# Performance work log

Hardware: AMD Instinct MI355X
Metric: run time of the kernel (lower is better)

Reference implementation:

```python
import jax, jax.numpy as jnp
import numpy as np
from jax import lax

B, V, M, C, CM, D = 48, 16, 32, 48, 8, 128
VOCAB_V, VOCAB_M, OUT = 2000, 1000, 256


def setup_inputs() -> dict:
    key = jax.random.key(0)
    ks = jax.random.split(key, 22)
    s = 0.1  # keep GRU gates out of saturation
    return {
        "visit_ids": jax.random.randint(ks[0], (3, B, V, C), 0, VOCAB_V),
        "mon_ids": jax.random.randint(ks[1], (4, B, V, M, CM), 0, VOCAB_M),
        "weight_vals": jax.random.uniform(ks[2], (B, V)),
        "age_vals": jax.random.uniform(ks[3], (B, V)),
        "emb_visit": jax.random.normal(ks[4], (3, VOCAB_V, D)) * s,
        "emb_mon": jax.random.normal(ks[5], (4, VOCAB_M, D)) * s,
        "mgru_Wih": jax.random.normal(ks[6], (5, 3 * D, D)) * s,
        "mgru_Whh": jax.random.normal(ks[7], (5, 3 * D, D)) * s,
        "mgru_bih": jax.random.normal(ks[8], (5, 3 * D)) * s,
        "mgru_bhh": jax.random.normal(ks[9], (5, 3 * D)) * s,
        "vgru_Wih": jax.random.normal(ks[10], (7, 3 * D, D)) * s,
        "vgru_Whh": jax.random.normal(ks[11], (7, 3 * D, D)) * s,
        "vgru_bih": jax.random.normal(ks[12], (7, 3 * D)) * s,
        "vgru_bhh": jax.random.normal(ks[13], (7, 3 * D)) * s,
        "fc_weight_w": jax.random.normal(ks[14], (D, 1)) * s,
        "fc_weight_b": jax.random.normal(ks[15], (D,)) * s,
        "fc_age_w": jax.random.normal(ks[16], (D, 1)) * s,
        "fc_age_b": jax.random.normal(ks[17], (D,)) * s,
        "fc_out_w": jax.random.normal(ks[18], (OUT, 7 * D)) * s,
        "fc_out_b": jax.random.normal(ks[19], (OUT,)) * s,
    }


def gru_last(x, Wih, Whh, bih, bhh):
    """torch.nn.GRU(batch_first=True), return final hidden [N, D]."""
    xi = jnp.einsum('ntd,ed->nte', x, Wih) + bih  # [N, T, 3D] input projections
    h0 = jnp.zeros((x.shape[0], Whh.shape[1]), x.dtype)

    def step(h, gi):
        gh = h @ Whh.T + bhh
        ir, iz, inn = jnp.split(gi, 3, axis=-1)
        hr, hz, hn = jnp.split(gh, 3, axis=-1)
        r = jax.nn.sigmoid(ir + hr)
        z = jax.nn.sigmoid(iz + hz)
        n = jnp.tanh(inn + r * hn)
        return (1.0 - z) * n + z * h, None

    hT, _ = lax.scan(step, h0, jnp.swapaxes(xi, 0, 1))
    return hT


def reference(visit_ids, mon_ids, weight_vals, age_vals, emb_visit, emb_mon,
              mgru_Wih, mgru_Whh, mgru_bih, mgru_bhh,
              vgru_Wih, vgru_Whh, vgru_bih, vgru_bhh,
              fc_weight_w, fc_weight_b, fc_age_w, fc_age_b,
              fc_out_w, fc_out_b):
    # padding_idx=0 -> zero embedding row (dropout in eval mode = identity)
    ev = emb_visit.at[:, 0].set(0.0)
    em = emb_mon.at[:, 0].set(0.0)

    # visit-event embedding-bag: sum over code dim -> [B, V, D] per feature
    visit_origin = [jnp.sum(ev[k][visit_ids[k]], axis=2) for k in range(3)]

    def run_stream(t, mi, vi):
        # monitor-level GRU over M, then visit-level GRU over V
        h1 = gru_last(t, mgru_Wih[mi], mgru_Whh[mi], mgru_bih[mi], mgru_bhh[mi])
        h2 = gru_last(h1.reshape(B, V, D),
                      vgru_Wih[vi], vgru_Whh[vi], vgru_bih[vi], vgru_bhh[vi])
        return h2  # [B, D]

    # output slots in dict-insertion order: lab_item, cond, proc, drug, inj_item, weight, age
    slots = [None] * 7
    for p in range(2):  # (lab_item, lab_value), (inj_item, inj_value)
        # elementwise item*value embedding, summed over codes -> [B*V, M, D]
        mon = jnp.sum(em[2 * p][mon_ids[2 * p]] * em[2 * p + 1][mon_ids[2 * p + 1]],
                      axis=3).reshape(B * V, M, D)
        slots[0 if p == 0 else 4] = run_stream(mon, p, p)
        for k in range(3):  # visit features repeated along monitor dim
            t = jnp.broadcast_to(visit_origin[k][:, :, None, :],
                                 (B, V, M, D)).reshape(B * V, M, D)
            h = run_stream(t, 2 + k, 2 + k)
            slots[1 + k] = h if slots[1 + k] is None else slots[1 + k] + h

    # weight / age: Linear(1->D), zero-mask, visit-level GRU
    for vals, w, b, vi, slot in ((weight_vals, fc_weight_w, fc_weight_b, 5, 5),
                                 (age_vals, fc_age_w, fc_age_b, 6, 6)):
        xf = vals.reshape(-1, 1)
        h = (xf @ w.T + b) * (xf != 0)
        slots[slot] = gru_last(h.reshape(B, V, D),
                               vgru_Wih[vi], vgru_Whh[vi], vgru_bih[vi], vgru_bhh[vi])

    patient_emb = jnp.concatenate(slots, axis=-1)  # [B, 7D]
    return jax.nn.relu(patient_emb) @ fc_out_w.T + fc_out_b
```

## Files before the change

### kernel.cpp

```cpp
#include <hip/hip_runtime.h>
#include <stdint.h>


typedef unsigned short u16;
typedef uint32_t u32;
typedef short bf8 __attribute__((ext_vector_type(8)));
typedef float f4 __attribute__((ext_vector_type(4)));

static __device__ __forceinline__ float bf2f(u16 b){ u32 u=((u32)b)<<16; float f; __builtin_memcpy(&f,&u,4); return f; }
static __device__ __forceinline__ u16 f2bf(float f){ u32 u; __builtin_memcpy(&u,&f,4); u32 r=(u+0x7fffu+((u>>16)&1u))>>16; return (u16)r; }
static __device__ __forceinline__ float bflo(u32 u){ u32 x=u<<16; float f; __builtin_memcpy(&f,&x,4); return f; }
static __device__ __forceinline__ float bfhi(u32 u){ u32 x=u&0xffff0000u; float f; __builtin_memcpy(&f,&x,4); return f; }
static __device__ __forceinline__ f4 mfma16(bf8 a, bf8 b, f4 c){ return __builtin_amdgcn_mfma_f32_16x16x32_bf16(a,b,c,0,0,0); }

#if __has_builtin(__builtin_amdgcn_exp2f)
static __device__ __forceinline__ float fexp2(float x){ return __builtin_amdgcn_exp2f(x); }
#else
static __device__ __forceinline__ float fexp2(float x){ float r; asm volatile("v_exp_f32 %0, %1" : "=v"(r) : "v"(x)); return r; }
#endif
#if __has_builtin(__builtin_amdgcn_rcpf)
static __device__ __forceinline__ float frcp(float x){ return __builtin_amdgcn_rcpf(x); }
#else
static __device__ __forceinline__ float frcp(float x){ float r; asm volatile("v_rcp_f32 %0, %1" : "=v"(r) : "v"(x)); return r; }
#endif

#define LOG2E 1.44269504089f
static __device__ __forceinline__ float sigm(float x){ return frcp(1.0f + fexp2(-LOG2E*x)); }
static __device__ __forceinline__ float tanh_f(float x){ return 1.0f - 2.0f*frcp(1.0f + fexp2((2.0f*LOG2E)*x)); }

__global__ __launch_bounds__(256) void k_prep(const float* __restrict__ s0, const float* __restrict__ s1,
                                              const float* __restrict__ s2, const float* __restrict__ s3,
                                              const float* __restrict__ s4,
                                              u16* __restrict__ d0, u16* __restrict__ d1,
                                              u16* __restrict__ d2, u16* __restrict__ d3,
                                              u16* __restrict__ d4){
  int y = blockIdx.y;
  const float* src = y==0?s0 : y==1?s1 : y==2?s2 : y==3?s3 : s4;
  u16* dst         = y==0?d0 : y==1?d1 : y==2?d2 : y==3?d3 : d4;
  int n4 = (y<2 ? 245760 : y<4 ? 344064 : 512000) >> 2;
  int i = blockIdx.x*256 + threadIdx.x;
  if (i < n4){
    float4 v = *(const float4*)(src + (size_t)i*4);
    ushort4 o = { f2bf(v.x), f2bf(v.y), f2bf(v.z), f2bf(v.w) };
    *(ushort4*)(dst + (size_t)i*4) = o;
  }
}

__global__ __launch_bounds__(128) void k_front(const int* __restrict__ vids,
                                               const float* __restrict__ embv,
                                               const float* __restrict__ wv, const float* __restrict__ av,
                                               const float* __restrict__ ww, const float* __restrict__ wb,
                                               const float* __restrict__ aw, const float* __restrict__ ab,
                                               u16* __restrict__ vis_org, u16* __restrict__ hin2T){
  __shared__ int ids[48];
  int y = blockIdx.y, row = blockIdx.x, d = threadIdx.x;
  if (y < 3){
    if (d < 48) ids[d] = vids[((size_t)y*768 + row)*48 + d];
    __syncthreads();
    const float* eb = embv + (size_t)y*2000*128;
    float acc = 0.f;
    #pragma unroll 4
    for (int c = 0; c < 48; ++c){ int id = ids[c]; if (id) acc += eb[(size_t)id*128 + d]; }
    vis_org[((size_t)y*768 + row)*128 + d] = f2bf(acc);
  } else {
    int sidx = y - 3;
    const float* vals = sidx ? av : wv;
    const float* wgt  = sidx ? aw : ww;
    const float* bias = sidx ? ab : wb;
    float v = vals[row];
    float h = (v != 0.f) ? (v * wgt[d] + bias[d]) : 0.f;
    int b = row >> 4, vv = row & 15;
    hin2T[((size_t)(5+sidx)*768 + (size_t)vv*48 + b)*128 + d] = f2bf(h);
  }
}

__global__ __launch_bounds__(256) void k_embed_mon(const int* __restrict__ mids,
                                                   const u16* __restrict__ embm_b,
                                                   u16* __restrict__ mon_xT){
  int p = blockIdx.y;
  int rid = threadIdx.x >> 5, lane32 = threadIdx.x & 31, d0 = lane32*4;
  __shared__ int ids[8][16];
  if (threadIdx.x < 128){
    int rr = threadIdx.x >> 4, c = threadIdx.x & 15;
    int f = 2*p + (c>>3), cm = c & 7;
    ids[rr][c] = mids[((size_t)f*24576 + (size_t)blockIdx.x*8 + rr)*8 + cm];
  }
  __syncthreads();
  const u16* e1 = embm_b + (size_t)(2*p)*1000*128;
  const u16* e2 = embm_b + (size_t)(2*p+1)*1000*128;
  float a0=0.f,a1=0.f,a2=0.f,a3=0.f;
  #pragma unroll
  for (int c = 0; c < 8; ++c){
    int i1 = ids[rid][c], i2 = ids[rid][8+c];
    if (i1 && i2){
      uint2 a = *(const uint2*)(e1 + (size_t)i1*128 + d0);
      uint2 b = *(const uint2*)(e2 + (size_t)i2*128 + d0);
      a0 += bflo(a.x)*bflo(b.x); a1 += bfhi(a.x)*bfhi(b.x);
      a2 += bflo(a.y)*bflo(b.y); a3 += bfhi(a.y)*bfhi(b.y);
    }
  }
  size_t nm = (size_t)blockIdx.x*8 + rid;
  int bv = (int)(nm >> 5), m = (int)(nm & 31);
  ushort4 o = { f2bf(a0), f2bf(a1), f2bf(a2), f2bf(a3) };
  *(ushort4*)(mon_xT + (size_t)p*24576*128 + ((size_t)m*768 + bv)*128 + d0) = o;
}


#define BARRIER() asm volatile("s_waitcnt lgkmcnt(0)\n\ts_barrier" ::: "memory")

#define ALOAD(D, tt) { int t_=(tt); if (t_>=T) t_=0; \
  const u16* p_ = ap + (size_t)t_*rstride; \
  D[0]=*(const bf8*)(p_); D[1]=*(const bf8*)(p_+32); \
  D[2]=*(const bf8*)(p_+64); D[3]=*(const bf8*)(p_+96); }

#define GIMM(G0,G1,G2,D) { \
  f4 t0_={biv[0],biv[0],biv[0],biv[0]}; G0=t0_; \
  f4 t1_={biv[1],biv[1],biv[1],biv[1]}; G1=t1_; \
  f4 t2_={biv[2],biv[2],biv[2],biv[2]}; G2=t2_; \
  G0=mfma16(D[0],wfi[0][0],G0); G0=mfma16(D[1],wfi[0][1],G0); \
  G0=mfma16(D[2],wfi[0][2],G0); G0=mfma16(D[3],wfi[0][3],G0); \
  G1=mfma16(D[0],wfi[1][0],G1); G1=mfma16(D[1],wfi[1][1],G1); \
  G1=mfma16(D[2],wfi[1][2],G1); G1=mfma16(D[3],wfi[1][3],G1); \
  G2=mfma16(D[0],wfi[2][0],G2); G2=mfma16(D[1],wfi[2][1],G2); \
  G2=mfma16(D[2],wfi[2][2],G2); G2=mfma16(D[3],wfi[2][3],G2); }

#define GHRD() \
  bf8 hf0_=*(const bf8*)&hlds[cur][lr][lq*8]; \
  bf8 hf1_=*(const bf8*)&hlds[cur][lr][32+lq*8]; \
  bf8 hf2_=*(const bf8*)&hlds[cur][lr][64+lq*8]; \
  bf8 hf3_=*(const bf8*)&hlds[cur][lr][96+lq*8]; \
  f4 a0_={bhv[0],bhv[0],bhv[0],bhv[0]}; \
  f4 a1_={bhv[1],bhv[1],bhv[1],bhv[1]}; \
  f4 a2_={bhv[2],bhv[2],bhv[2],bhv[2]}; \
  a0_=mfma16(hf0_,wfh[0][0],a0_); a0_=mfma16(hf1_,wfh[0][1],a0_); \
  a0_=mfma16(hf2_,wfh[0][2],a0_); a0_=mfma16(hf3_,wfh[0][3],a0_); \
  a1_=mfma16(hf0_,wfh[1][0],a1_); a1_=mfma16(hf1_,wfh[1][1],a1_); \
  a1_=mfma16(hf2_,wfh[1][2],a1_); a1_=mfma16(hf3_,wfh[1][3],a1_); \
  a2_=mfma16(hf0_,wfh[2][0],a2_); a2_=mfma16(hf1_,wfh[2][1],a2_); \
  a2_=mfma16(hf2_,wfh[2][2],a2_); a2_=mfma16(hf3_,wfh[2][3],a2_);

#define GATES(G0,G1,G2) { int nxt_=cur^1; \
  _Pragma("unroll") \
  for (int r=0;r<4;++r){ \
    float rr_=sigm(G0[r]+a0_[r]); \
    float zz_=sigm(G1[r]+a1_[r]); \
    float nn_=tanh_f(G2[r]+rr_*a2_[r]); \
    float hv_=(1.0f-zz_)*nn_+zz_*hp[r]; hp[r]=hv_; \
    hlds[nxt_][lq*4+r][w*16+lr]=f2bf(hv_); } \
  BARRIER(); cur=nxt_; }

#define STEP0(G0,G1,G2) { \
  f4 a0_={bhv[0],bhv[0],bhv[0],bhv[0]}; \
  f4 a1_={bhv[1],bhv[1],bhv[1],bhv[1]}; \
  f4 a2_={bhv[2],bhv[2],bhv[2],bhv[2]}; \
  GATES(G0,G1,G2); }

#define STEPB(G0,G1,G2,SN,tt) { \
  GHRD(); \
  GATES(G0,G1,G2); \
  if ((tt)+2 < T){ GIMM(G0,G1,G2,SN); } \
  ALOAD(SN,(tt)+4); }

__global__ __launch_bounds__(512, 2) void k_gru(int mode,
    const u16* __restrict__ Asrc, const u16* __restrict__ Asrc2,
    const u16* __restrict__ Wih, const float* __restrict__ bih,
    const u16* __restrict__ Whh, const float* __restrict__ bhh,
    u16* __restrict__ hout, int T){
  int s = blockIdx.y, g = blockIdx.x;
  const u16* A; size_t rstride; u16* ho; int widx;
  if (mode == 0){
    if (s < 2){ A = Asrc + (size_t)s*24576*128; rstride = 768*128; }
    else      { A = Asrc2 + (size_t)(s-2)*768*128; rstride = 0; }
    widx = s;
    int slot = (0x32140u >> (4*s)) & 15;
    ho = hout + (size_t)slot*768*128;
  } else {
    A = Asrc + (size_t)s*768*128; rstride = 48*128;
    widx = (0x6514320u >> (4*s)) & 15;
    ho = hout + (size_t)s*48*128;
  }
  const u16* Wi = Wih + (size_t)widx*384*128;
  const u16* Wh = Whh + (size_t)widx*384*128;
  const float* bi = bih + (size_t)widx*384;
  const float* bh = bhh + (size_t)widx*384;

  int w = threadIdx.x >> 6, l = threadIdx.x & 63;
  int lr = l & 15, lq = l >> 4;

  bf8 wfi[3][4], wfh[3][4]; float biv[3], bhv[3];
  #pragma unroll
  for (int j = 0; j < 3; ++j){
    int colb = (w + 8*j)*16;
    const u16* wpi = Wi + (size_t)(colb + lr)*128 + lq*8;
    const u16* wph = Wh + (size_t)(colb + lr)*128 + lq*8;
    #pragma unroll
    for (int kt = 0; kt < 4; ++kt){
      wfi[j][kt] = *(const bf8*)(wpi + kt*32);
      wfh[j][kt] = *(const bf8*)(wph + kt*32);
    }
    biv[j] = bi[colb + lr];
    bhv[j] = bh[colb + lr];
  }

  const u16* ap = A + (size_t)(g*16 + lr)*128 + lq*8;
  __shared__ u16 hlds[2][16][132];
  float hp[4] = {0.f,0.f,0.f,0.f};
  int cur = 0;

  if (rstride){
    bf8 S0[4], S1[4];
    f4 gE0,gE1,gE2, gO0,gO1,gO2;
    ALOAD(S0,0); ALOAD(S1,1);
    GIMM(gE0,gE1,gE2,S0); ALOAD(S0,2);
    GIMM(gO0,gO1,gO2,S1); ALOAD(S1,3);
    STEP0(gE0,gE1,gE2);
    GIMM(gE0,gE1,gE2,S0); ALOAD(S0,4);
    STEPB(gO0,gO1,gO2,S1,1);
    for (int t = 2; t < T; t += 2){
      STEPB(gE0,gE1,gE2,S0,t);
      STEPB(gO0,gO1,gO2,S1,t+1);
    }
  } else {
    bf8 S0[4];
    f4 gE0,gE1,gE2;
    ALOAD(S0,0);
    GIMM(gE0,gE1,gE2,S0);
    STEP0(gE0,gE1,gE2);
    for (int t = 1; t < T; ++t){
      GHRD();
      GATES(gE0,gE1,gE2);
    }
  }

  if (mode == 0){
    #pragma unroll
    for (int r = 0; r < 4; ++r)
      ho[((size_t)(lq*4+r)*48 + g)*128 + w*16 + lr] = f2bf(hp[r]);
  } else {
    #pragma unroll
    for (int r = 0; r < 4; ++r)
      ho[((size_t)(g*16 + lq*4 + r))*128 + w*16 + lr] = f2bf(hp[r]);
  }
}

__global__ __launch_bounds__(256) void k_final(const u16* __restrict__ h2,
                                               const float* __restrict__ W,
                                               const float* __restrict__ Bias,
                                               float* __restrict__ out){
  int b = blockIdx.x, t = threadIdx.x;
  __shared__ float emb[896];
  for (int i = t; i < 896; i += 256){
    int j = i >> 7, d = i & 127;
    float v = bf2f(h2[((size_t)j*48 + b)*128 + d]);
    if (j >= 1 && j <= 3) v *= 2.0f;
    emb[i] = fmaxf(v, 0.f);
  }
  __syncthreads();
  float acc = Bias[t];
  const float* wp = W + (size_t)t*896;
  for (int i = 0; i < 896; i += 8){
    float4 w0 = *(const float4*)(wp + i);
    float4 w1 = *(const float4*)(wp + i + 4);
    acc += w0.x*emb[i]   + w0.y*emb[i+1] + w0.z*emb[i+2] + w0.w*emb[i+3];
    acc += w1.x*emb[i+4] + w1.y*emb[i+5] + w1.z*emb[i+6] + w1.w*emb[i+7];
  }
  out[(size_t)b*256 + t] = acc;
}

extern "C" void kernel_launch(void* const* d_in, const int* in_sizes, int n_in,
                              void* d_out, int out_size, void* d_ws, size_t ws_size,
                              hipStream_t stream){
  const int*   visit_ids   = (const int*)d_in[0];
  const int*   mon_ids     = (const int*)d_in[1];
  const float* weight_vals = (const float*)d_in[2];
  const float* age_vals    = (const float*)d_in[3];
  const float* emb_visit   = (const float*)d_in[4];
  const float* emb_mon     = (const float*)d_in[5];
  const float* mgru_Wih    = (const float*)d_in[6];
  const float* mgru_Whh    = (const float*)d_in[7];
  const float* mgru_bih    = (const float*)d_in[8];
  const float* mgru_bhh    = (const float*)d_in[9];
  const float* vgru_Wih    = (const float*)d_in[10];
  const float* vgru_Whh    = (const float*)d_in[11];
  const float* vgru_bih    = (const float*)d_in[12];
  const float* vgru_bhh    = (const float*)d_in[13];
  const float* fc_w_w      = (const float*)d_in[14];
  const float* fc_w_b      = (const float*)d_in[15];
  const float* fc_a_w      = (const float*)d_in[16];
  const float* fc_a_b      = (const float*)d_in[17];
  const float* fc_out_w    = (const float*)d_in[18];
  const float* fc_out_b    = (const float*)d_in[19];

  char* ws = (char*)d_ws;
  size_t o = 0;
  u16* mWih_b  = (u16*)(ws+o); o += 5ull*384*128*2;
  u16* mWhh_b  = (u16*)(ws+o); o += 5ull*384*128*2;
  u16* vWih_b  = (u16*)(ws+o); o += 7ull*384*128*2;
  u16* vWhh_b  = (u16*)(ws+o); o += 7ull*384*128*2;
  u16* embm_b  = (u16*)(ws+o); o += 4ull*1000*128*2;
  u16* mon_xT  = (u16*)(ws+o); o += 2ull*24576*128*2;
  u16* vis_org = (u16*)(ws+o); o += 3ull*768*128*2;
  u16* hin2T   = (u16*)(ws+o); o += 7ull*768*128*2;
  u16* h2      = (u16*)(ws+o); o += 7ull*48*128*2;

  k_prep<<<dim3(500,5), 256, 0, stream>>>(mgru_Wih, mgru_Whh, vgru_Wih, vgru_Whh, emb_mon,
                                          mWih_b, mWhh_b, vWih_b, vWhh_b, embm_b);
  k_front<<<dim3(768,5), 128, 0, stream>>>(visit_ids, emb_visit,
                                           weight_vals, age_vals, fc_w_w, fc_w_b, fc_a_w, fc_a_b,
                                           vis_org, hin2T);
  k_embed_mon<<<dim3(3072,2), 256, 0, stream>>>(mon_ids, embm_b, mon_xT);
  k_gru<<<dim3(48,5), 512, 0, stream>>>(0, mon_xT, vis_org,
                                        mWih_b, mgru_bih, mWhh_b, mgru_bhh, hin2T, 32);
  k_gru<<<dim3(3,7), 512, 0, stream>>>(1, hin2T, (const u16*)0,
                                       vWih_b, vgru_bih, vWhh_b, vgru_bhh, h2, 16);
  k_final<<<48, 256, 0, stream>>>(h2, fc_out_w, fc_out_b, (float*)d_out);
}
```

Before: 132.9 us.

## Fuse front-end kernels and interleave two GRU groups per block

Merges the weight-conversion, visit-embedding, scalar-feature and monitor-embedding kernels into one launch. The monitor embedding now reads fp32 tables directly instead of first writing a bf16 copy. Each GRU block now advances two independent 16-row recurrences in lockstep, so the MFMA and transcendental latency of one chain can hide behind the other. The weight and age visit-level GRUs also run inside the first GRU launch rather than waiting for the second. The cost is half as many GRU blocks, more registers per block, and duplicated work when the last group index is clamped.

```diff
diff --git a/kernel.cpp b/kernel.cpp
--- a/kernel.cpp
+++ b/kernel.cpp
@@ -9,8 +9,6 @@
 
 static __device__ __forceinline__ float bf2f(u16 b){ u32 u=((u32)b)<<16; float f; __builtin_memcpy(&f,&u,4); return f; }
 static __device__ __forceinline__ u16 f2bf(float f){ u32 u; __builtin_memcpy(&u,&f,4); u32 r=(u+0x7fffu+((u>>16)&1u))>>16; return (u16)r; }
-static __device__ __forceinline__ float bflo(u32 u){ u32 x=u<<16; float f; __builtin_memcpy(&f,&x,4); return f; }
-static __device__ __forceinline__ float bfhi(u32 u){ u32 x=u&0xffff0000u; float f; __builtin_memcpy(&f,&x,4); return f; }
 static __device__ __forceinline__ f4 mfma16(bf8 a, bf8 b, f4 c){ return __builtin_amdgcn_mfma_f32_16x16x32_bf16(a,b,c,0,0,0); }
 
 #if __has_builtin(__builtin_amdgcn_exp2f)
@@ -23,166 +21,183 @@
 #else
 static __device__ __forceinline__ float frcp(float x){ float r; asm volatile("v_rcp_f32 %0, %1" : "=v"(r) : "v"(x)); return r; }
 #endif
-
 #define LOG2E 1.44269504089f
 static __device__ __forceinline__ float sigm(float x){ return frcp(1.0f + fexp2(-LOG2E*x)); }
 static __device__ __forceinline__ float tanh_f(float x){ return 1.0f - 2.0f*frcp(1.0f + fexp2((2.0f*LOG2E)*x)); }
 
-__global__ __launch_bounds__(256) void k_prep(const float* __restrict__ s0, const float* __restrict__ s1,
-                                              const float* __restrict__ s2, const float* __restrict__ s3,
-                                              const float* __restrict__ s4,
-                                              u16* __restrict__ d0, u16* __restrict__ d1,
-                                              u16* __restrict__ d2, u16* __restrict__ d3,
-                                              u16* __restrict__ d4){
+__global__ __launch_bounds__(256) void k_pre(const int* __restrict__ vids, const int* __restrict__ mids,
+    const float* __restrict__ embv, const float* __restrict__ embm,
+    const float* __restrict__ wv, const float* __restrict__ av,
+    const float* __restrict__ ww, const float* __restrict__ wb,
+    const float* __restrict__ aw, const float* __restrict__ ab,
+    const float* __restrict__ mWih_f, const float* __restrict__ mWhh_f,
+    const float* __restrict__ vWih_f, const float* __restrict__ vWhh_f,
+    u16* __restrict__ mWih_b, u16* __restrict__ mWhh_b,
+    u16* __restrict__ vWih_b, u16* __restrict__ vWhh_b,
+    u16* __restrict__ mon_xT, u16* __restrict__ vis_org, u16* __restrict__ hin2T){
   int y = blockIdx.y;
-  const float* src = y==0?s0 : y==1?s1 : y==2?s2 : y==3?s3 : s4;
-  u16* dst         = y==0?d0 : y==1?d1 : y==2?d2 : y==3?d3 : d4;
-  int n4 = (y<2 ? 245760 : y<4 ? 344064 : 512000) >> 2;
-  int i = blockIdx.x*256 + threadIdx.x;
-  if (i < n4){
-    float4 v = *(const float4*)(src + (size_t)i*4);
+  if (y < 2){
+    int p = y;
+    int rid = threadIdx.x >> 5, lane32 = threadIdx.x & 31, d0 = lane32*4;
+    __shared__ int ids[8][16];
+    if (threadIdx.x < 128){
+      int rr = threadIdx.x >> 4, c = threadIdx.x & 15;
+      int f = 2*p + (c>>3), cm = c & 7;
+      ids[rr][c] = mids[((size_t)f*24576 + (size_t)blockIdx.x*8 + rr)*8 + cm];
+    }
+    __syncthreads();
+    const float* e1 = embm + (size_t)(2*p)*1000*128;
+    const float* e2 = embm + (size_t)(2*p+1)*1000*128;
+    float a0=0.f,a1=0.f,a2=0.f,a3=0.f;
+    #pragma unroll
+    for (int c = 0; c < 8; ++c){
+      int i1 = ids[rid][c], i2 = ids[rid][8+c];
+      if (i1 && i2){
+        float4 a = *(const float4*)(e1 + (size_t)i1*128 + d0);
+        float4 b = *(const float4*)(e2 + (size_t)i2*128 + d0);
+        a0 += a.x*b.x; a1 += a.y*b.y; a2 += a.z*b.z; a3 += a.w*b.w;
+      }
+    }
+    size_t nm = (size_t)blockIdx.x*8 + rid;
+    int bv = (int)(nm >> 5), m = (int)(nm & 31);
+    ushort4 o = { f2bf(a0), f2bf(a1), f2bf(a2), f2bf(a3) };
+    *(ushort4*)(mon_xT + (size_t)p*24576*128 + ((size_t)m*768 + bv)*128 + d0) = o;
+  } else if (y == 2){
+    int i = blockIdx.x*256 + threadIdx.x;
+    if (i >= 294912) return;
+    const float* s; u16* d; int off;
+    if (i < 61440)      { s = mWih_f; d = mWih_b; off = i; }
+    else if (i < 122880){ s = mWhh_f; d = mWhh_b; off = i - 61440; }
+    else if (i < 208896){ s = vWih_f; d = vWih_b; off = i - 122880; }
+    else                { s = vWhh_f; d = vWhh_b; off = i - 208896; }
+    float4 v = *(const float4*)(s + (size_t)off*4);
     ushort4 o = { f2bf(v.x), f2bf(v.y), f2bf(v.z), f2bf(v.w) };
-    *(ushort4*)(dst + (size_t)i*4) = o;
+    *(ushort4*)(d + (size_t)off*4) = o;
+  } else {
+    int x = blockIdx.x;
+    int sub = threadIdx.x >> 7, d = threadIdx.x & 127;
+    if (x < 1152){
+      __shared__ int ids[2][48];
+      int row = x*2 + sub;
+      int k = row / 768, bv = row - k*768;
+      if (d < 48) ids[sub][d] = vids[((size_t)k*768 + bv)*48 + d];
+      __syncthreads();
+      const float* eb = embv + (size_t)k*2000*128;
+      float acc = 0.f;
+      #pragma unroll 4
+      for (int c = 0; c < 48; ++c){ int id = ids[sub][c]; if (id) acc += eb[(size_t)id*128 + d]; }
+      vis_org[((size_t)k*768 + bv)*128 + d] = f2bf(acc);
+    } else if (x < 1920){
+      int grow = (x - 1152)*2 + sub;
+      int sidx = grow >= 768 ? 1 : 0;
+      int row = grow - sidx*768;
+      const float* vals = sidx ? av : wv;
+      const float* wgt  = sidx ? aw : ww;
+      const float* bias = sidx ? ab : wb;
+      float v = vals[row];
+      float h = (v != 0.f) ? (v * wgt[d] + bias[d]) : 0.f;
+      int b = row >> 4, vv = row & 15;
+      hin2T[((size_t)(5+sidx)*768 + (size_t)vv*48 + b)*128 + d] = f2bf(h);
+    }
   }
 }
 
-__global__ __launch_bounds__(128) void k_front(const int* __restrict__ vids,
-                                               const float* __restrict__ embv,
-                                               const float* __restrict__ wv, const float* __restrict__ av,
-                                               const float* __restrict__ ww, const float* __restrict__ wb,
-                                               const float* __restrict__ aw, const float* __restrict__ ab,
-                                               u16* __restrict__ vis_org, u16* __restrict__ hin2T){
-  __shared__ int ids[48];
-  int y = blockIdx.y, row = blockIdx.x, d = threadIdx.x;
-  if (y < 3){
-    if (d < 48) ids[d] = vids[((size_t)y*768 + row)*48 + d];
-    __syncthreads();
-    const float* eb = embv + (size_t)y*2000*128;
-    float acc = 0.f;
-    #pragma unroll 4
-    for (int c = 0; c < 48; ++c){ int id = ids[c]; if (id) acc += eb[(size_t)id*128 + d]; }
-    vis_org[((size_t)y*768 + row)*128 + d] = f2bf(acc);
-  } else {
-    int sidx = y - 3;
-    const float* vals = sidx ? av : wv;
-    const float* wgt  = sidx ? aw : ww;
-    const float* bias = sidx ? ab : wb;
-    float v = vals[row];
-    float h = (v != 0.f) ? (v * wgt[d] + bias[d]) : 0.f;
-    int b = row >> 4, vv = row & 15;
-    hin2T[((size_t)(5+sidx)*768 + (size_t)vv*48 + b)*128 + d] = f2bf(h);
-  }
-}
-
-__global__ __launch_bounds__(256) void k_embed_mon(const int* __restrict__ mids,
-                                                   const u16* __restrict__ embm_b,
-                                                   u16* __restrict__ mon_xT){
-  int p = blockIdx.y;
-  int rid = threadIdx.x >> 5, lane32 = threadIdx.x & 31, d0 = lane32*4;
-  __shared__ int ids[8][16];
-  if (threadIdx.x < 128){
-    int rr = threadIdx.x >> 4, c = threadIdx.x & 15;
-    int f = 2*p + (c>>3), cm = c & 7;
-    ids[rr][c] = mids[((size_t)f*24576 + (size_t)blockIdx.x*8 + rr)*8 + cm];
-  }
-  __syncthreads();
-  const u16* e1 = embm_b + (size_t)(2*p)*1000*128;
-  const u16* e2 = embm_b + (size_t)(2*p+1)*1000*128;
-  float a0=0.f,a1=0.f,a2=0.f,a3=0.f;
-  #pragma unroll
-  for (int c = 0; c < 8; ++c){
-    int i1 = ids[rid][c], i2 = ids[rid][8+c];
-    if (i1 && i2){
-      uint2 a = *(const uint2*)(e1 + (size_t)i1*128 + d0);
-      uint2 b = *(const uint2*)(e2 + (size_t)i2*128 + d0);
-      a0 += bflo(a.x)*bflo(b.x); a1 += bfhi(a.x)*bfhi(b.x);
-      a2 += bflo(a.y)*bflo(b.y); a3 += bfhi(a.y)*bfhi(b.y);
-    }
-  }
-  size_t nm = (size_t)blockIdx.x*8 + rid;
-  int bv = (int)(nm >> 5), m = (int)(nm & 31);
-  ushort4 o = { f2bf(a0), f2bf(a1), f2bf(a2), f2bf(a3) };
-  *(ushort4*)(mon_xT + (size_t)p*24576*128 + ((size_t)m*768 + bv)*128 + d0) = o;
-}
-
 
 #define BARRIER() asm volatile("s_waitcnt lgkmcnt(0)\n\ts_barrier" ::: "memory")
 
-#define ALOAD(D, tt) { int t_=(tt); if (t_>=T) t_=0; \
+#define ALOADg(S, ap, tt) { int t_=(tt); if (t_>=T) t_=0; \
   const u16* p_ = ap + (size_t)t_*rstride; \
-  D[0]=*(const bf8*)(p_); D[1]=*(const bf8*)(p_+32); \
-  D[2]=*(const bf8*)(p_+64); D[3]=*(const bf8*)(p_+96); }
-
-#define GIMM(G0,G1,G2,D) { \
+  S[0]=*(const bf8*)(p_); S[1]=*(const bf8*)(p_+32); \
+  S[2]=*(const bf8*)(p_+64); S[3]=*(const bf8*)(p_+96); }
+
+#define GIMMg(G0,G1,G2,S) { \
   f4 t0_={biv[0],biv[0],biv[0],biv[0]}; G0=t0_; \
   f4 t1_={biv[1],biv[1],biv[1],biv[1]}; G1=t1_; \
   f4 t2_={biv[2],biv[2],biv[2],biv[2]}; G2=t2_; \
-  G0=mfma16(D[0],wfi[0][0],G0); G0=mfma16(D[1],wfi[0][1],G0); \
-  G0=mfma16(D[2],wfi[0][2],G0); G0=mfma16(D[3],wfi[0][3],G0); \
-  G1=mfma16(D[0],wfi[1][0],G1); G1=mfma16(D[1],wfi[1][1],G1); \
-  G1=mfma16(D[2],wfi[1][2],G1); G1=mfma16(D[3],wfi[1][3],G1); \
-  G2=mfma16(D[0],wfi[2][0],G2); G2=mfma16(D[1],wfi[2][1],G2); \
-  G2=mfma16(D[2],wfi[2][2],G2); G2=mfma16(D[3],wfi[2][3],G2); }
-
-#define GHRD() \
-  bf8 hf0_=*(const bf8*)&hlds[cur][lr][lq*8]; \
-  bf8 hf1_=*(const bf8*)&hlds[cur][lr][32+lq*8]; \
-  bf8 hf2_=*(const bf8*)&hlds[cur][lr][64+lq*8]; \
-  bf8 hf3_=*(const bf8*)&hlds[cur][lr][96+lq*8]; \
-  f4 a0_={bhv[0],bhv[0],bhv[0],bhv[0]}; \
-  f4 a1_={bhv[1],bhv[1],bhv[1],bhv[1]}; \
-  f4 a2_={bhv[2],bhv[2],bhv[2],bhv[2]}; \
-  a0_=mfma16(hf0_,wfh[0][0],a0_); a0_=mfma16(hf1_,wfh[0][1],a0_); \
-  a0_=mfma16(hf2_,wfh[0][2],a0_); a0_=mfma16(hf3_,wfh[0][3],a0_); \
-  a1_=mfma16(hf0_,wfh[1][0],a1_); a1_=mfma16(hf1_,wfh[1][1],a1_); \
-  a1_=mfma16(hf2_,wfh[1][2],a1_); a1_=mfma16(hf3_,wfh[1][3],a1_); \
-  a2_=mfma16(hf0_,wfh[2][0],a2_); a2_=mfma16(hf1_,wfh[2][1],a2_); \
-  a2_=mfma16(hf2_,wfh[2][2],a2_); a2_=mfma16(hf3_,wfh[2][3],a2_);
-
-#define GATES(G0,G1,G2) { int nxt_=cur^1; \
+  G0=mfma16(S[0],wfi[0][0],G0); G0=mfma16(S[1],wfi[0][1],G0); \
+  G0=mfma16(S[2],wfi[0][2],G0); G0=mfma16(S[3],wfi[0][3],G0); \
+  G1=mfma16(S[0],wfi[1][0],G1); G1=mfma16(S[1],wfi[1][1],G1); \
+  G1=mfma16(S[2],wfi[1][2],G1); G1=mfma16(S[3],wfi[1][3],G1); \
+  G2=mfma16(S[0],wfi[2][0],G2); G2=mfma16(S[1],wfi[2][1],G2); \
+  G2=mfma16(S[2],wfi[2][2],G2); G2=mfma16(S[3],wfi[2][3],G2); }
+
+#define GHRDg(a0,a1,a2,grp) { \
+  bf8 hf0_=*(const bf8*)&hlds[cur][grp][lr][lq*8]; \
+  bf8 hf1_=*(const bf8*)&hlds[cur][grp][lr][32+lq*8]; \
+  bf8 hf2_=*(const bf8*)&hlds[cur][grp][lr][64+lq*8]; \
+  bf8 hf3_=*(const bf8*)&hlds[cur][grp][lr][96+lq*8]; \
+  f4 i0_={bhv[0],bhv[0],bhv[0],bhv[0]}; a0=i0_; \
+  f4 i1_={bhv[1],bhv[1],bhv[1],bhv[1]}; a1=i1_; \
+  f4 i2_={bhv[2],bhv[2],bhv[2],bhv[2]}; a2=i2_; \
+  a0=mfma16(hf0_,wfh[0][0],a0); a0=mfma16(hf1_,wfh[0][1],a0); \
+  a0=mfma16(hf2_,wfh[0][2],a0); a0=mfma16(hf3_,wfh[0][3],a0); \
+  a1=mfma16(hf0_,wfh[1][0],a1); a1=mfma16(hf1_,wfh[1][1],a1); \
+  a1=mfma16(hf2_,wfh[1][2],a1); a1=mfma16(hf3_,wfh[1][3],a1); \
+  a2=mfma16(hf0_,wfh[2][0],a2); a2=mfma16(hf1_,wfh[2][1],a2); \
+  a2=mfma16(hf2_,wfh[2][2],a2); a2=mfma16(hf3_,wfh[2][3],a2); }
+
+#define GATESg(G0,G1,G2,a0,a1,a2,hp,grp,nxt) { \
   _Pragma("unroll") \
   for (int r=0;r<4;++r){ \
-    float rr_=sigm(G0[r]+a0_[r]); \
-    float zz_=sigm(G1[r]+a1_[r]); \
-    float nn_=tanh_f(G2[r]+rr_*a2_[r]); \
+    float rr_=sigm(G0[r]+a0[r]); \
+    float zz_=sigm(G1[r]+a1[r]); \
+    float nn_=tanh_f(G2[r]+rr_*a2[r]); \
     float hv_=(1.0f-zz_)*nn_+zz_*hp[r]; hp[r]=hv_; \
-    hlds[nxt_][lq*4+r][w*16+lr]=f2bf(hv_); } \
+    hlds[nxt][grp][lq*4+r][w*16+lr]=f2bf(hv_); } }
+
+#define STEP0P() { int nxt_=cur^1; \
+  f4 aA0={bhv[0],bhv[0],bhv[0],bhv[0]}, aA1={bhv[1],bhv[1],bhv[1],bhv[1]}, aA2={bhv[2],bhv[2],bhv[2],bhv[2]}; \
+  f4 aB0=aA0, aB1=aA1, aB2=aA2; \
+  GATESg(eA0,eA1,eA2,aA0,aA1,aA2,hpA,0,nxt_); \
+  GATESg(eB0,eB1,eB2,aB0,aB1,aB2,hpB,1,nxt_); \
   BARRIER(); cur=nxt_; }
 
-#define STEP0(G0,G1,G2) { \
-  f4 a0_={bhv[0],bhv[0],bhv[0],bhv[0]}; \
-  f4 a1_={bhv[1],bhv[1],bhv[1],bhv[1]}; \
-  f4 a2_={bhv[2],bhv[2],bhv[2],bhv[2]}; \
-  GATES(G0,G1,G2); }
-
-#define STEPB(G0,G1,G2,SN,tt) { \
-  GHRD(); \
-  GATES(G0,G1,G2); \
-  if ((tt)+2 < T){ GIMM(G0,G1,G2,SN); } \
-  ALOAD(SN,(tt)+4); }
-
-__global__ __launch_bounds__(512, 2) void k_gru(int mode,
-    const u16* __restrict__ Asrc, const u16* __restrict__ Asrc2,
-    const u16* __restrict__ Wih, const float* __restrict__ bih,
-    const u16* __restrict__ Whh, const float* __restrict__ bhh,
-    u16* __restrict__ hout, int T){
-  int s = blockIdx.y, g = blockIdx.x;
-  const u16* A; size_t rstride; u16* ho; int widx;
-  if (mode == 0){
-    if (s < 2){ A = Asrc + (size_t)s*24576*128; rstride = 768*128; }
-    else      { A = Asrc2 + (size_t)(s-2)*768*128; rstride = 0; }
-    widx = s;
+#define STEPP(GA0,GA1,GA2,GB0,GB1,GB2,tt) { int nxt_=cur^1; \
+  f4 aA0,aA1,aA2,aB0,aB1,aB2; \
+  GHRDg(aA0,aA1,aA2,0); \
+  GHRDg(aB0,aB1,aB2,1); \
+  GATESg(GA0,GA1,GA2,aA0,aA1,aA2,hpA,0,nxt_); \
+  GATESg(GB0,GB1,GB2,aB0,aB1,aB2,hpB,1,nxt_); \
+  BARRIER(); cur=nxt_; \
+  if ((tt)+2 < T){ GIMMg(GA0,GA1,GA2,SA); GIMMg(GB0,GB1,GB2,SB); } \
+  ALOADg(SA,apA,(tt)+3); ALOADg(SB,apB,(tt)+3); }
+
+#define STEPC() { int nxt_=cur^1; \
+  f4 aA0,aA1,aA2,aB0,aB1,aB2; \
+  GHRDg(aA0,aA1,aA2,0); \
+  GHRDg(aB0,aB1,aB2,1); \
+  GATESg(eA0,eA1,eA2,aA0,aA1,aA2,hpA,0,nxt_); \
+  GATESg(eB0,eB1,eB2,aB0,aB1,aB2,hpB,1,nxt_); \
+  BARRIER(); cur=nxt_; }
+
+__global__ __launch_bounds__(512, 2) void k_gru(int phase,
+    const u16* __restrict__ mon_xT, const u16* __restrict__ vis_org,
+    u16* __restrict__ hin2T, u16* __restrict__ h2,
+    const u16* __restrict__ mWih, const float* __restrict__ mbih,
+    const u16* __restrict__ mWhh, const float* __restrict__ mbhh,
+    const u16* __restrict__ vWih, const float* __restrict__ vbih,
+    const u16* __restrict__ vWhh, const float* __restrict__ vbhh){
+  int s = blockIdx.y;
+  const u16* A; size_t rstride; int T, oMode, gA, gB;
+  const u16 *Wi, *Wh; const float *bi2, *bh2; u16* ho;
+  bool vjob = (phase == 1) || (s >= 5);
+  if (!vjob){
+    T = 32; oMode = 0; gA = 2*blockIdx.x; gB = gA + 1;
+    if (s < 2){ A = mon_xT + (size_t)s*24576*128; rstride = 768*128; }
+    else      { A = vis_org + (size_t)(s-2)*768*128; rstride = 0; }
+    Wi = mWih + (size_t)s*49152; Wh = mWhh + (size_t)s*49152;
+    bi2 = mbih + (size_t)s*384;  bh2 = mbhh + (size_t)s*384;
     int slot = (0x32140u >> (4*s)) & 15;
-    ho = hout + (size_t)slot*768*128;
+    ho = hin2T + (size_t)slot*768*128;
   } else {
-    A = Asrc + (size_t)s*768*128; rstride = 48*128;
-    widx = (0x6514320u >> (4*s)) & 15;
-    ho = hout + (size_t)s*48*128;
-  }
-  const u16* Wi = Wih + (size_t)widx*384*128;
-  const u16* Wh = Whh + (size_t)widx*384*128;
-  const float* bi = bih + (size_t)widx*384;
-  const float* bh = bhh + (size_t)widx*384;
+    if (blockIdx.x >= 2) return;
+    T = 16; oMode = 1; gA = 2*blockIdx.x; gB = gA + 1; if (gB > 2) gB = 2;
+    A = hin2T + (size_t)s*768*128; rstride = 48*128;
+    int vi = (0x6514320u >> (4*s)) & 15;
+    Wi = vWih + (size_t)vi*49152; Wh = vWhh + (size_t)vi*49152;
+    bi2 = vbih + (size_t)vi*384;  bh2 = vbhh + (size_t)vi*384;
+    ho = h2 + (size_t)s*48*128;
+  }
 
   int w = threadIdx.x >> 6, l = threadIdx.x & 63;
   int lr = l & 15, lq = l >> 4;
@@ -198,48 +213,53 @@
       wfi[j][kt] = *(const bf8*)(wpi + kt*32);
       wfh[j][kt] = *(const bf8*)(wph + kt*32);
     }
-    biv[j] = bi[colb + lr];
-    bhv[j] = bh[colb + lr];
-  }
-
-  const u16* ap = A + (size_t)(g*16 + lr)*128 + lq*8;
-  __shared__ u16 hlds[2][16][132];
-  float hp[4] = {0.f,0.f,0.f,0.f};
+    biv[j] = bi2[colb + lr];
+    bhv[j] = bh2[colb + lr];
+  }
+
+  const u16* apA = A + (size_t)(gA*16 + lr)*128 + lq*8;
+  const u16* apB = A + (size_t)(gB*16 + lr)*128 + lq*8;
+  __shared__ u16 hlds[2][2][16][132];
+  float hpA[4] = {0.f,0.f,0.f,0.f}, hpB[4] = {0.f,0.f,0.f,0.f};
   int cur = 0;
 
   if (rstride){
-    bf8 S0[4], S1[4];
-    f4 gE0,gE1,gE2, gO0,gO1,gO2;
-    ALOAD(S0,0); ALOAD(S1,1);
-    GIMM(gE0,gE1,gE2,S0); ALOAD(S0,2);
-    GIMM(gO0,gO1,gO2,S1); ALOAD(S1,3);
-    STEP0(gE0,gE1,gE2);
-    GIMM(gE0,gE1,gE2,S0); ALOAD(S0,4);
-    STEPB(gO0,gO1,gO2,S1,1);
+    bf8 SA[4], SB[4];
+    f4 eA0,eA1,eA2, oA0,oA1,oA2, eB0,eB1,eB2, oB0,oB1,oB2;
+    ALOADg(SA,apA,0); ALOADg(SB,apB,0);
+    GIMMg(eA0,eA1,eA2,SA); GIMMg(eB0,eB1,eB2,SB);
+    ALOADg(SA,apA,1); ALOADg(SB,apB,1);
+    GIMMg(oA0,oA1,oA2,SA); GIMMg(oB0,oB1,oB2,SB);
+    ALOADg(SA,apA,2); ALOADg(SB,apB,2);
+    STEP0P();
+    GIMMg(eA0,eA1,eA2,SA); GIMMg(eB0,eB1,eB2,SB);
+    ALOADg(SA,apA,3); ALOADg(SB,apB,3);
+    STEPP(oA0,oA1,oA2,oB0,oB1,oB2,1);
     for (int t = 2; t < T; t += 2){
-      STEPB(gE0,gE1,gE2,S0,t);
-      STEPB(gO0,gO1,gO2,S1,t+1);
+      STEPP(eA0,eA1,eA2,eB0,eB1,eB2,t);
+      STEPP(oA0,oA1,oA2,oB0,oB1,oB2,t+1);
     }
   } else {
-    bf8 S0[4];
-    f4 gE0,gE1,gE2;
-    ALOAD(S0,0);
-    GIMM(gE0,gE1,gE2,S0);
-    STEP0(gE0,gE1,gE2);
-    for (int t = 1; t < T; ++t){
-      GHRD();
-      GATES(gE0,gE1,gE2);
-    }
-  }
-
-  if (mode == 0){
+    bf8 SA[4], SB[4];
+    f4 eA0,eA1,eA2, eB0,eB1,eB2;
+    ALOADg(SA,apA,0); ALOADg(SB,apB,0);
+    GIMMg(eA0,eA1,eA2,SA); GIMMg(eB0,eB1,eB2,SB);
+    STEP0P();
+    for (int t = 1; t < T; ++t) STEPC();
+  }
+
+  if (oMode == 0){
     #pragma unroll
-    for (int r = 0; r < 4; ++r)
-      ho[((size_t)(lq*4+r)*48 + g)*128 + w*16 + lr] = f2bf(hp[r]);
+    for (int r = 0; r < 4; ++r){
+      ho[((size_t)(lq*4+r)*48 + gA)*128 + w*16 + lr] = f2bf(hpA[r]);
+      ho[((size_t)(lq*4+r)*48 + gB)*128 + w*16 + lr] = f2bf(hpB[r]);
+    }
   } else {
     #pragma unroll
-    for (int r = 0; r < 4; ++r)
-      ho[((size_t)(g*16 + lq*4 + r))*128 + w*16 + lr] = f2bf(hp[r]);
+    for (int r = 0; r < 4; ++r){
+      ho[((size_t)(gA*16 + lq*4 + r))*128 + w*16 + lr] = f2bf(hpA[r]);
+      ho[((size_t)(gB*16 + lq*4 + r))*128 + w*16 + lr] = f2bf(hpB[r]);
+    }
   }
 }
 
@@ -297,21 +317,19 @@
   u16* mWhh_b  = (u16*)(ws+o); o += 5ull*384*128*2;
   u16* vWih_b  = (u16*)(ws+o); o += 7ull*384*128*2;
   u16* vWhh_b  = (u16*)(ws+o); o += 7ull*384*128*2;
-  u16* embm_b  = (u16*)(ws+o); o += 4ull*1000*128*2;
   u16* mon_xT  = (u16*)(ws+o); o += 2ull*24576*128*2;
   u16* vis_org = (u16*)(ws+o); o += 3ull*768*128*2;
   u16* hin2T   = (u16*)(ws+o); o += 7ull*768*128*2;
   u16* h2      = (u16*)(ws+o); o += 7ull*48*128*2;
 
-  k_prep<<<dim3(500,5), 256, 0, stream>>>(mgru_Wih, mgru_Whh, vgru_Wih, vgru_Whh, emb_mon,
-                                          mWih_b, mWhh_b, vWih_b, vWhh_b, embm_b);
-  k_front<<<dim3(768,5), 128, 0, stream>>>(visit_ids, emb_visit,
-                                           weight_vals, age_vals, fc_w_w, fc_w_b, fc_a_w, fc_a_b,
-                                           vis_org, hin2T);
-  k_embed_mon<<<dim3(3072,2), 256, 0, stream>>>(mon_ids, embm_b, mon_xT);
-  k_gru<<<dim3(48,5), 512, 0, stream>>>(0, mon_xT, vis_org,
-                                        mWih_b, mgru_bih, mWhh_b, mgru_bhh, hin2T, 32);
-  k_gru<<<dim3(3,7), 512, 0, stream>>>(1, hin2T, (const u16*)0,
-                                       vWih_b, vgru_bih, vWhh_b, vgru_bhh, h2, 16);
+  k_pre<<<dim3(3072,4), 256, 0, stream>>>(visit_ids, mon_ids, emb_visit, emb_mon,
+      weight_vals, age_vals, fc_w_w, fc_w_b, fc_a_w, fc_a_b,
+      mgru_Wih, mgru_Whh, vgru_Wih, vgru_Whh,
+      mWih_b, mWhh_b, vWih_b, vWhh_b,
+      mon_xT, vis_org, hin2T);
+  k_gru<<<dim3(24,7), 512, 0, stream>>>(0, mon_xT, vis_org, hin2T, h2,
+      mWih_b, mgru_bih, mWhh_b, mgru_bhh, vWih_b, vgru_bih, vWhh_b, vgru_bhh);
+  k_gru<<<dim3(2,5), 512, 0, stream>>>(1, mon_xT, vis_org, hin2T, h2,
+      mWih_b, mgru_bih, mWhh_b, mgru_bhh, vWih_b, vgru_bih, vWhh_b, vgru_bhh);
   k_final<<<48, 256, 0, stream>>>(h2, fc_out_w, fc_out_b, (float*)d_out);
 }
```

After: 194.4 us. 46.2% more time.
